# Kernel optimization log

Hardware: AMD Instinct MI355X
Metric: run time of the kernel (lower is better)

Reference implementation:

```python
import jax, jax.numpy as jnp
import numpy as np

OBS_LEN = 20
IN_DIM = 64
HID_DIM = 128
BATCH = 65536


def setup_inputs() -> dict:
    key = jax.random.key(0)
    ks = jax.random.split(key, 9)
    s_emb = 1.0 / np.sqrt(2.0)
    s_lstm = 1.0 / np.sqrt(HID_DIM)
    return {
        "obs_goal": jax.random.normal(ks[0], (OBS_LEN, BATCH, 2), dtype=jnp.float32),
        "h0": jax.random.normal(ks[1], (BATCH, HID_DIM), dtype=jnp.float32),
        "c0": jax.random.normal(ks[2], (BATCH, HID_DIM), dtype=jnp.float32),
        "W_emb": jax.random.uniform(ks[3], (IN_DIM, 2), jnp.float32, -s_emb, s_emb),
        "b_emb": jax.random.uniform(ks[4], (IN_DIM,), jnp.float32, -s_emb, s_emb),
        "W_ih": jax.random.uniform(ks[5], (4 * HID_DIM, IN_DIM), jnp.float32, -s_lstm, s_lstm),
        "W_hh": jax.random.uniform(ks[6], (4 * HID_DIM, HID_DIM), jnp.float32, -s_lstm, s_lstm),
        "b_ih": jax.random.uniform(ks[7], (4 * HID_DIM,), jnp.float32, -s_lstm, s_lstm),
        "b_hh": jax.random.uniform(ks[8], (4 * HID_DIM,), jnp.float32, -s_lstm, s_lstm),
    }


def reference(obs_goal, h0, c0, W_emb, b_emb, W_ih, W_hh, b_ih, b_hh):
    # input embedding: [T*B, 2] @ [2, D] -> [T, B, D]
    T, B, _ = obs_goal.shape
    x_emb = (obs_goal.reshape(-1, 2) @ W_emb.T + b_emb).reshape(T, B, IN_DIM)

    def step(carry, x_t):
        h, c = carry
        # gates: [B, 4H], torch LSTMCell chunk order = (i, f, g, o)
        gates = x_t @ W_ih.T + b_ih + h @ W_hh.T + b_hh
        i, f, g, o = jnp.split(gates, 4, axis=-1)
        i = jax.nn.sigmoid(i)
        f = jax.nn.sigmoid(f)
        g = jnp.tanh(g)
        o = jax.nn.sigmoid(o)
        c_new = f * c + i * g
        h_new = o * jnp.tanh(c_new)
        return (h_new, c_new), None

    (h_final, _), _ = jax.lax.scan(step, (h0, c0), x_emb[:OBS_LEN])
    return h_final
```

## Files before the change

### kernel.cpp

```cpp
#include <hip/hip_runtime.h>

#define OBS_T 20
#define HID 128
#define NGATE 512
#define MB 32
#define HSTR 136

typedef __bf16 bf16x8 __attribute__((ext_vector_type(8)));
typedef __bf16 bf16x4 __attribute__((ext_vector_type(4)));
typedef float f32x4 __attribute__((ext_vector_type(4)));

__device__ __forceinline__ float fast_rcp(float x) { return __builtin_amdgcn_rcpf(x); }
#if __has_builtin(__builtin_amdgcn_exp2f)
__device__ __forceinline__ float exp2_hw(float x) { return __builtin_amdgcn_exp2f(x); }
#else
__device__ __forceinline__ float exp2_hw(float x) { return __expf(x * 0.69314718056f); }
#endif
#define LOG2E 1.442695041f

__global__ void prep_vec(const float* __restrict__ W_emb, const float* __restrict__ b_emb,
                         const float* __restrict__ W_ih, const float* __restrict__ b_ih,
                         const float* __restrict__ b_hh,
                         float* __restrict__ biasp, float* __restrict__ wx0p,
                         float* __restrict__ wx1p) {
  int r = blockIdx.x * blockDim.x + threadIdx.x;
  if (r >= NGATE) return;
  float s0 = 0.f, s1 = 0.f, sb = 0.f;
  for (int d = 0; d < 64; ++d) {
    float w = W_ih[r * 64 + d];
    s0 += w * W_emb[d * 2 + 0];
    s1 += w * W_emb[d * 2 + 1];
    sb += w * b_emb[d];
  }
  int q = r >> 7, j = r & 127;
  int np = (j >> 4) * 64 + q * 16 + (j & 15);
  biasp[np] = b_ih[r] + b_hh[r] + sb;
  wx0p[np] = s0;
  wx1p[np] = s1;
}

__global__ void prep_wp(const float* __restrict__ W_hh, __bf16* __restrict__ Wp) {
  int tid = blockIdx.x * blockDim.x + threadIdx.x;
  int jj = tid & 7;
  int lane = (tid >> 3) & 63;
  int frag = tid >> 9;
  int ks = frag & 3;
  int q = (frag >> 2) & 3;
  int w = frag >> 4;
  int cn = lane & 15, quad = lane >> 4;
  int r = q * 128 + w * 16 + cn;
  int k = ks * 32 + quad * 8 + jj;
  Wp[tid] = (__bf16)W_hh[r * 128 + k];
}

__device__ __forceinline__ float cell_update(float gi, float gf, float gg, float go,
                                             float& c) {
  float e_i = exp2_hw(gi * -LOG2E);
  float e_f = exp2_hw(gf * -LOG2E);
  float e_g = exp2_hw(gg * (-2.f * LOG2E));
  float e_o = exp2_hw(go * -LOG2E);
  float rf = fast_rcp(1.f + e_f);
  float ig = (1.f - e_g) * fast_rcp((1.f + e_i) * (1.f + e_g));
  c = fmaf(rf, c, ig);
  float e_c = exp2_hw(c * (-2.f * LOG2E));
  return (1.f - e_c) * fast_rcp((1.f + e_o) * (1.f + e_c));
}

__global__ __launch_bounds__(512, 2) void lstm_fused(
    const float* __restrict__ obs, const float* __restrict__ h0,
    const float* __restrict__ c0, const __bf16* __restrict__ Wp,
    const float* __restrict__ biasp, const float* __restrict__ wx0p,
    const float* __restrict__ wx1p, float* __restrict__ out, int batch) {
  __shared__ __align__(16) __bf16 hbuf[2][MB][HSTR];
  __shared__ __align__(16) float obs_s[OBS_T][MB][2];

  const int tid = threadIdx.x;
  const int lane = tid & 63;
  const int wv = tid >> 6;
  const int cn = lane & 15;
  const int quad = lane >> 4;
  const int bbase = blockIdx.x * MB;
  const int junit = wv * 16 + cn;

  if (tid < OBS_T * MB * 2 / 4) {
    const int t = tid >> 4, f4 = tid & 15;
    ((float4*)obs_s)[tid] = ((const float4*)obs)[(t * batch + bbase) / 2 + f4];
  }
#pragma unroll
  for (int it = 0; it < 2; ++it) {
    int idx = tid + it * 512;
    int row = idx >> 5, c4 = idx & 31;
    float4 v = ((const float4*)h0)[(bbase + row) * 32 + c4];
    bf16x4 b;
    b.x = (__bf16)v.x; b.y = (__bf16)v.y; b.z = (__bf16)v.z; b.w = (__bf16)v.w;
    *(bf16x4*)&hbuf[0][row][c4 * 4] = b;
  }

  bf16x8 Bf[4][4];
  {
    const bf16x8* wp8 = (const bf16x8*)Wp;
#pragma unroll
    for (int q = 0; q < 4; ++q)
#pragma unroll
      for (int ks = 0; ks < 4; ++ks)
        Bf[ks][q] = wp8[(wv * 16 + q * 4 + ks) * 64 + lane];
  }

  float bias_v[4], wx0_v[4], wx1_v[4];
#pragma unroll
  for (int q = 0; q < 4; ++q) {
    int n = wv * 64 + q * 16 + cn;
    bias_v[q] = biasp[n];
    wx0_v[q] = wx0p[n];
    wx1_v[q] = wx1p[n];
  }

  float cc[2][4];
#pragma unroll
  for (int s = 0; s < 2; ++s)
#pragma unroll
    for (int r = 0; r < 4; ++r)
      cc[s][r] = c0[(bbase + s * 16 + quad * 4 + r) * HID + junit];

  __syncthreads();

  int cur = 0;
#pragma unroll 1
  for (int t = 0; t < OBS_T - 1; ++t) {
    f32x4 acc[2][4];
#pragma unroll
    for (int s = 0; s < 2; ++s)
#pragma unroll
      for (int r = 0; r < 4; ++r) {
        float2 ob = *(const float2*)&obs_s[t][s * 16 + quad * 4 + r][0];
#pragma unroll
        for (int q = 0; q < 4; ++q)
          acc[s][q][r] = fmaf(ob.y, wx1_v[q], fmaf(ob.x, wx0_v[q], bias_v[q]));
      }

#pragma unroll
    for (int ks = 0; ks < 4; ++ks) {
      bf16x8 Av0 = *(const bf16x8*)&hbuf[cur][cn][ks * 32 + quad * 8];
      bf16x8 Av1 = *(const bf16x8*)&hbuf[cur][16 + cn][ks * 32 + quad * 8];
#pragma unroll
      for (int q = 0; q < 4; ++q) {
        acc[0][q] = __builtin_amdgcn_mfma_f32_16x16x32_bf16(Av0, Bf[ks][q], acc[0][q], 0, 0, 0);
        acc[1][q] = __builtin_amdgcn_mfma_f32_16x16x32_bf16(Av1, Bf[ks][q], acc[1][q], 0, 0, 0);
      }
    }

    const int nxt = cur ^ 1;
#pragma unroll
    for (int s = 0; s < 2; ++s)
#pragma unroll
      for (int r = 0; r < 4; ++r) {
        float h = cell_update(acc[s][0][r], acc[s][1][r], acc[s][2][r], acc[s][3][r],
                              cc[s][r]);
        hbuf[nxt][s * 16 + quad * 4 + r][junit] = (__bf16)h;
      }
    __syncthreads();
    cur = nxt;
  }

  {
    const int t = OBS_T - 1;
    f32x4 acc[2][4];
#pragma unroll
    for (int s = 0; s < 2; ++s)
#pragma unroll
      for (int r = 0; r < 4; ++r) {
        float2 ob = *(const float2*)&obs_s[t][s * 16 + quad * 4 + r][0];
#pragma unroll
        for (int q = 0; q < 4; ++q)
          acc[s][q][r] = fmaf(ob.y, wx1_v[q], fmaf(ob.x, wx0_v[q], bias_v[q]));
      }
#pragma unroll
    for (int ks = 0; ks < 4; ++ks) {
      bf16x8 Av0 = *(const bf16x8*)&hbuf[cur][cn][ks * 32 + quad * 8];
      bf16x8 Av1 = *(const bf16x8*)&hbuf[cur][16 + cn][ks * 32 + quad * 8];
#pragma unroll
      for (int q = 0; q < 4; ++q) {
        acc[0][q] = __builtin_amdgcn_mfma_f32_16x16x32_bf16(Av0, Bf[ks][q], acc[0][q], 0, 0, 0);
        acc[1][q] = __builtin_amdgcn_mfma_f32_16x16x32_bf16(Av1, Bf[ks][q], acc[1][q], 0, 0, 0);
      }
    }
#pragma unroll
    for (int s = 0; s < 2; ++s)
#pragma unroll
      for (int r = 0; r < 4; ++r) {
        float h = cell_update(acc[s][0][r], acc[s][1][r], acc[s][2][r], acc[s][3][r],
                              cc[s][r]);
        out[(bbase + s * 16 + quad * 4 + r) * HID + junit] = h;
      }
  }
}

extern "C" void kernel_launch(void* const* d_in, const int* in_sizes, int n_in,
                              void* d_out, int out_size, void* d_ws, size_t ws_size,
                              hipStream_t stream) {
  const float* obs = (const float*)d_in[0];
  const float* h0 = (const float*)d_in[1];
  const float* c0 = (const float*)d_in[2];
  const float* W_emb = (const float*)d_in[3];
  const float* b_emb = (const float*)d_in[4];
  const float* W_ih = (const float*)d_in[5];
  const float* W_hh = (const float*)d_in[6];
  const float* b_ih = (const float*)d_in[7];
  const float* b_hh = (const float*)d_in[8];
  float* out = (float*)d_out;
  const int batch = in_sizes[1] / HID;

  __bf16* Wp = (__bf16*)d_ws;
  float* biasp = (float*)((char*)d_ws + 131072);
  float* wx0p = biasp + NGATE;
  float* wx1p = wx0p + NGATE;

  prep_vec<<<2, 256, 0, stream>>>(W_emb, b_emb, W_ih, b_ih, b_hh, biasp, wx0p, wx1p);
  prep_wp<<<256, 256, 0, stream>>>(W_hh, Wp);
  lstm_fused<<<batch / MB, 512, 0, stream>>>(obs, h0, c0, Wp, biasp, wx0p, wx1p, out, batch);
}
```

Before: 405.4 us.

## Halve batch tile to 16 rows with 4 waves each owning two hidden slices

Each block now covers 16 batch rows with 256 threads (4 waves) instead of 32 rows with 512 threads. Each wave keeps two column-groups of W_hh fragments in registers and reuses one A fragment across both, so every block runs its own step-to-step barrier and twice as many blocks exist. The cell update is also rewritten to use a single reciprocal for the c update, trading it for a few extra multiplies. The risks are doubled register use for weights, which can lower occupancy, and more total weight loads across the larger number of blocks.

Result: slower. 500.2 us (+23.4%).

```diff
diff --git a/kernel.cpp b/kernel.cpp
--- a/kernel.cpp
+++ b/kernel.cpp
@@ -3,7 +3,7 @@
 #define OBS_T 20
 #define HID 128
 #define NGATE 512
-#define MB 32
+#define MB 16
 #define HSTR 136
 
 typedef __bf16 bf16x8 __attribute__((ext_vector_type(8)));
@@ -46,9 +46,9 @@
   int frag = tid >> 9;
   int ks = frag & 3;
   int q = (frag >> 2) & 3;
-  int w = frag >> 4;
+  int g16 = frag >> 4;
   int cn = lane & 15, quad = lane >> 4;
-  int r = q * 128 + w * 16 + cn;
+  int r = q * 128 + g16 * 16 + cn;
   int k = ks * 32 + quad * 8 + jj;
   Wp[tid] = (__bf16)W_hh[r * 128 + k];
 }
@@ -59,14 +59,17 @@
   float e_f = exp2_hw(gf * -LOG2E);
   float e_g = exp2_hw(gg * (-2.f * LOG2E));
   float e_o = exp2_hw(go * -LOG2E);
-  float rf = fast_rcp(1.f + e_f);
-  float ig = (1.f - e_g) * fast_rcp((1.f + e_i) * (1.f + e_g));
-  c = fmaf(rf, c, ig);
+  float a_i = 1.f + e_i, a_f = 1.f + e_f, a_g = 1.f + e_g;
+  float m1 = a_i * a_g;
+  float r = fast_rcp(m1 * a_f);
+  float t = fmaf(c, m1, (2.f - a_g) * a_f);
+  c = t * r;
   float e_c = exp2_hw(c * (-2.f * LOG2E));
-  return (1.f - e_c) * fast_rcp((1.f + e_o) * (1.f + e_c));
-}
-
-__global__ __launch_bounds__(512, 2) void lstm_fused(
+  float a_c = 1.f + e_c;
+  return (2.f - a_c) * fast_rcp((1.f + e_o) * a_c);
+}
+
+__global__ __launch_bounds__(256, 2) void lstm_fused(
     const float* __restrict__ obs, const float* __restrict__ h0,
     const float* __restrict__ c0, const __bf16* __restrict__ Wp,
     const float* __restrict__ biasp, const float* __restrict__ wx0p,
@@ -80,15 +83,16 @@
   const int cn = lane & 15;
   const int quad = lane >> 4;
   const int bbase = blockIdx.x * MB;
-  const int junit = wv * 16 + cn;
+  const int ju0 = (wv * 2) * 16 + cn;
+  const int ju1 = ju0 + 16;
 
   if (tid < OBS_T * MB * 2 / 4) {
-    const int t = tid >> 4, f4 = tid & 15;
+    const int t = tid >> 3, f4 = tid & 7;
     ((float4*)obs_s)[tid] = ((const float4*)obs)[(t * batch + bbase) / 2 + f4];
   }
 #pragma unroll
   for (int it = 0; it < 2; ++it) {
-    int idx = tid + it * 512;
+    int idx = tid + it * 256;
     int row = idx >> 5, c4 = idx & 31;
     float4 v = ((const float4*)h0)[(bbase + row) * 32 + c4];
     bf16x4 b;
@@ -96,31 +100,35 @@
     *(bf16x4*)&hbuf[0][row][c4 * 4] = b;
   }
 
-  bf16x8 Bf[4][4];
+  bf16x8 Bf[2][4][4];
   {
     const bf16x8* wp8 = (const bf16x8*)Wp;
 #pragma unroll
-    for (int q = 0; q < 4; ++q)
-#pragma unroll
-      for (int ks = 0; ks < 4; ++ks)
-        Bf[ks][q] = wp8[(wv * 16 + q * 4 + ks) * 64 + lane];
-  }
-
-  float bias_v[4], wx0_v[4], wx1_v[4];
-#pragma unroll
-  for (int q = 0; q < 4; ++q) {
-    int n = wv * 64 + q * 16 + cn;
-    bias_v[q] = biasp[n];
-    wx0_v[q] = wx0p[n];
-    wx1_v[q] = wx1p[n];
-  }
+    for (int u = 0; u < 2; ++u)
+#pragma unroll
+      for (int q = 0; q < 4; ++q)
+#pragma unroll
+        for (int ks = 0; ks < 4; ++ks)
+          Bf[u][ks][q] = wp8[((wv * 2 + u) * 16 + q * 4 + ks) * 64 + lane];
+  }
+
+  float bias_v[2][4], wx0_v[2][4], wx1_v[2][4];
+#pragma unroll
+  for (int u = 0; u < 2; ++u)
+#pragma unroll
+    for (int q = 0; q < 4; ++q) {
+      int n = (wv * 2 + u) * 64 + q * 16 + cn;
+      bias_v[u][q] = biasp[n];
+      wx0_v[u][q] = wx0p[n];
+      wx1_v[u][q] = wx1p[n];
+    }
 
   float cc[2][4];
 #pragma unroll
-  for (int s = 0; s < 2; ++s)
-#pragma unroll
-    for (int r = 0; r < 4; ++r)
-      cc[s][r] = c0[(bbase + s * 16 + quad * 4 + r) * HID + junit];
+  for (int r = 0; r < 4; ++r) {
+    cc[0][r] = c0[(bbase + quad * 4 + r) * HID + ju0];
+    cc[1][r] = c0[(bbase + quad * 4 + r) * HID + ju1];
+  }
 
   __syncthreads();
 
@@ -129,35 +137,33 @@
   for (int t = 0; t < OBS_T - 1; ++t) {
     f32x4 acc[2][4];
 #pragma unroll
-    for (int s = 0; s < 2; ++s)
-#pragma unroll
-      for (int r = 0; r < 4; ++r) {
-        float2 ob = *(const float2*)&obs_s[t][s * 16 + quad * 4 + r][0];
+    for (int r = 0; r < 4; ++r) {
+      float2 ob = *(const float2*)&obs_s[t][quad * 4 + r][0];
+#pragma unroll
+      for (int u = 0; u < 2; ++u)
 #pragma unroll
         for (int q = 0; q < 4; ++q)
-          acc[s][q][r] = fmaf(ob.y, wx1_v[q], fmaf(ob.x, wx0_v[q], bias_v[q]));
+          acc[u][q][r] = fmaf(ob.y, wx1_v[u][q], fmaf(ob.x, wx0_v[u][q], bias_v[u][q]));
+    }
+
+#pragma unroll
+    for (int ks = 0; ks < 4; ++ks) {
+      bf16x8 Av = *(const bf16x8*)&hbuf[cur][cn][ks * 32 + quad * 8];
+#pragma unroll
+      for (int q = 0; q < 4; ++q) {
+        acc[0][q] = __builtin_amdgcn_mfma_f32_16x16x32_bf16(Av, Bf[0][ks][q], acc[0][q], 0, 0, 0);
+        acc[1][q] = __builtin_amdgcn_mfma_f32_16x16x32_bf16(Av, Bf[1][ks][q], acc[1][q], 0, 0, 0);
       }
-
-#pragma unroll
-    for (int ks = 0; ks < 4; ++ks) {
-      bf16x8 Av0 = *(const bf16x8*)&hbuf[cur][cn][ks * 32 + quad * 8];
-      bf16x8 Av1 = *(const bf16x8*)&hbuf[cur][16 + cn][ks * 32 + quad * 8];
-#pragma unroll
-      for (int q = 0; q < 4; ++q) {
-        acc[0][q] = __builtin_amdgcn_mfma_f32_16x16x32_bf16(Av0, Bf[ks][q], acc[0][q], 0, 0, 0);
-        acc[1][q] = __builtin_amdgcn_mfma_f32_16x16x32_bf16(Av1, Bf[ks][q], acc[1][q], 0, 0, 0);
-      }
     }
 
     const int nxt = cur ^ 1;
 #pragma unroll
-    for (int s = 0; s < 2; ++s)
-#pragma unroll
-      for (int r = 0; r < 4; ++r) {
-        float h = cell_update(acc[s][0][r], acc[s][1][r], acc[s][2][r], acc[s][3][r],
-                              cc[s][r]);
-        hbuf[nxt][s * 16 + quad * 4 + r][junit] = (__bf16)h;
-      }
+    for (int r = 0; r < 4; ++r) {
+      float h0v = cell_update(acc[0][0][r], acc[0][1][r], acc[0][2][r], acc[0][3][r], cc[0][r]);
+      float h1v = cell_update(acc[1][0][r], acc[1][1][r], acc[1][2][r], acc[1][3][r], cc[1][r]);
+      hbuf[nxt][quad * 4 + r][ju0] = (__bf16)h0v;
+      hbuf[nxt][quad * 4 + r][ju1] = (__bf16)h1v;
+    }
     __syncthreads();
     cur = nxt;
   }
@@ -166,32 +172,30 @@
     const int t = OBS_T - 1;
     f32x4 acc[2][4];
 #pragma unroll
-    for (int s = 0; s < 2; ++s)
-#pragma unroll
-      for (int r = 0; r < 4; ++r) {
-        float2 ob = *(const float2*)&obs_s[t][s * 16 + quad * 4 + r][0];
+    for (int r = 0; r < 4; ++r) {
+      float2 ob = *(const float2*)&obs_s[t][quad * 4 + r][0];
+#pragma unroll
+      for (int u = 0; u < 2; ++u)
 #pragma unroll
         for (int q = 0; q < 4; ++q)
-          acc[s][q][r] = fmaf(ob.y, wx1_v[q], fmaf(ob.x, wx0_v[q], bias_v[q]));
+          acc[u][q][r] = fmaf(ob.y, wx1_v[u][q], fmaf(ob.x, wx0_v[u][q], bias_v[u][q]));
+    }
+#pragma unroll
+    for (int ks = 0; ks < 4; ++ks) {
+      bf16x8 Av = *(const bf16x8*)&hbuf[cur][cn][ks * 32 + quad * 8];
+#pragma unroll
+      for (int q = 0; q < 4; ++q) {
+        acc[0][q] = __builtin_amdgcn_mfma_f32_16x16x32_bf16(Av, Bf[0][ks][q], acc[0][q], 0, 0, 0);
+        acc[1][q] = __builtin_amdgcn_mfma_f32_16x16x32_bf16(Av, Bf[1][ks][q], acc[1][q], 0, 0, 0);
       }
-#pragma unroll
-    for (int ks = 0; ks < 4; ++ks) {
-      bf16x8 Av0 = *(const bf16x8*)&hbuf[cur][cn][ks * 32 + quad * 8];
-      bf16x8 Av1 = *(const bf16x8*)&hbuf[cur][16 + cn][ks * 32 + quad * 8];
-#pragma unroll
-      for (int q = 0; q < 4; ++q) {
-        acc[0][q] = __builtin_amdgcn_mfma_f32_16x16x32_bf16(Av0, Bf[ks][q], acc[0][q], 0, 0, 0);
-        acc[1][q] = __builtin_amdgcn_mfma_f32_16x16x32_bf16(Av1, Bf[ks][q], acc[1][q], 0, 0, 0);
-      }
-    }
-#pragma unroll
-    for (int s = 0; s < 2; ++s)
-#pragma unroll
-      for (int r = 0; r < 4; ++r) {
-        float h = cell_update(acc[s][0][r], acc[s][1][r], acc[s][2][r], acc[s][3][r],
-                              cc[s][r]);
-        out[(bbase + s * 16 + quad * 4 + r) * HID + junit] = h;
-      }
+    }
+#pragma unroll
+    for (int r = 0; r < 4; ++r) {
+      float h0v = cell_update(acc[0][0][r], acc[0][1][r], acc[0][2][r], acc[0][3][r], cc[0][r]);
+      float h1v = cell_update(acc[1][0][r], acc[1][1][r], acc[1][2][r], acc[1][3][r], cc[1][r]);
+      out[(bbase + quad * 4 + r) * HID + ju0] = h0v;
+      out[(bbase + quad * 4 + r) * HID + ju1] = h1v;
+    }
   }
 }
 
@@ -217,5 +221,5 @@
 
   prep_vec<<<2, 256, 0, stream>>>(W_emb, b_emb, W_ih, b_ih, b_hh, biasp, wx0p, wx1p);
   prep_wp<<<256, 256, 0, stream>>>(W_hh, Wp);
-  lstm_fused<<<batch / MB, 512, 0, stream>>>(obs, h0, c0, Wp, biasp, wx0p, wx1p, out, batch);
-}
+  lstm_fused<<<batch / MB, 256, 0, stream>>>(obs, h0, c0, Wp, biasp, wx0p, wx1p, out, batch);
+}
```
